# Optimization experiments

Hardware: AMD Instinct MI355X
Metric: run time of the kernel (lower is better)

Reference implementation:

```python
import jax, jax.numpy as jnp
import numpy as np

B, T, V, E, H, O = 64, 512, 32000, 512, 512, 1

def setup_inputs() -> dict:
    key = jax.random.key(0)
    ks = jax.random.split(key, 6)
    s = 0.02  # small init scale to keep gates unsaturated
    return {
        "input_words": jax.random.randint(ks[0], (B, T), 0, V, dtype=jnp.int64),
        "emb": jax.random.normal(ks[1], (V, E), jnp.float32) * s,
        "Wi": jax.random.normal(ks[2], (E, 4 * H), jnp.float32) * s,
        "bi": jnp.zeros((4 * H,), jnp.float32),
        "Wh": jax.random.normal(ks[3], (H, 4 * H), jnp.float32) * s,
        "bh": jnp.zeros((4 * H,), jnp.float32),
        "W_lstm": jax.random.normal(ks[4], (H, H), jnp.float32) * s,
        "b_lstm": jnp.zeros((H,), jnp.float32),
        "W_att": jax.random.normal(ks[5], (2 * H, O), jnp.float32) * s,
        "b_att": jnp.zeros((O,), jnp.float32),
    }


def reference(input_words, emb, Wi, bi, Wh, bh, W_lstm, b_lstm, W_att, b_att):
    batch, seq_len = input_words.shape
    x = emb[input_words]                                  # [B,T,E]
    # precompute all input-side gate projections (r,f,g,o stacked)
    xp = jnp.einsum('bte,eg->tbg', x, Wi) + bi            # [T,B,4H]

    h0 = jnp.zeros((batch, H), xp.dtype)
    c0 = jnp.zeros((batch, H), xp.dtype)

    def step(carry, xp_t):
        h, c = carry
        gates = xp_t + h @ Wh + bh                        # [B,4H]
        r, f, g, o = jnp.split(gates, 4, axis=-1)
        rt = jax.nn.sigmoid(r)
        ft = jax.nn.sigmoid(f)
        gt = jnp.tanh(g)
        ot = jax.nn.sigmoid(o)
        c = ft * c + rt * gt
        h = ot * jnp.tanh(c)
        return (h, c), h

    (h, c), hs = jax.lax.scan(step, (h0, c0), xp)         # hs: [T,B,H]
    outputs = hs.transpose(1, 0, 2)                       # [B,T,H]

    final_hidden = h @ W_lstm + b_lstm                    # [B,H]
    score = jnp.einsum('bth,bh->bt', outputs, final_hidden)
    dist = jax.nn.softmax(score, axis=-1)                 # torch Softmax() -> dim=1 on 2D
    att = jnp.einsum('bth,bt->bh', outputs, dist)
    out = jnp.concatenate([final_hidden, att], axis=1) @ W_att + b_att
    return jax.nn.sigmoid(out), h
```

## Files before the change

kernel.cpp:

```cpp
#include <hip/hip_runtime.h>
#include <hip/hip_bf16.h>

#define BB 64
#define TT 512
#define EE 512
#define HH 512
#define G4 2048
#define VV 32000
#define NWG 64

typedef float f32x4 __attribute__((ext_vector_type(4)));
typedef short s16x8 __attribute__((ext_vector_type(8)));
typedef unsigned short u16x8 __attribute__((ext_vector_type(8)));

__device__ __forceinline__ unsigned short f2bf(float x) {
    __hip_bfloat16 h = __float2bfloat16(x);
    return *(unsigned short*)&h;
}
__device__ __forceinline__ float b2f(unsigned short u) {
    return __uint_as_float(((unsigned)u) << 16);
}

__global__ __launch_bounds__(256) void c_bf16(const float* __restrict__ in,
                                              unsigned short* __restrict__ out, int n4) {
    int i = blockIdx.x * 256 + threadIdx.x;
    if (i < n4) {
        float4 v = ((const float4*)in)[i];
        ushort4 o;
        o.x = f2bf(v.x); o.y = f2bf(v.y); o.z = f2bf(v.z); o.w = f2bf(v.w);
        ((ushort4*)out)[i] = o;
    }
}

__global__ __launch_bounds__(256) void c_wT(const float* __restrict__ in,
                                            unsigned short* __restrict__ out) {
    __shared__ float tile[32][33];
    int gx = blockIdx.x * 32;
    int ky = blockIdx.y * 32;
    int tx = threadIdx.x & 31, ty = threadIdx.x >> 5;
    #pragma unroll
    for (int i = 0; i < 32; i += 8)
        tile[ty + i][tx] = in[(size_t)(ky + ty + i) * G4 + gx + tx];
    __syncthreads();
    #pragma unroll
    for (int i = 0; i < 32; i += 8)
        out[(size_t)(gx + ty + i) * HH + ky + tx] = f2bf(tile[tx][ty + i]);
}

__global__ void zero_flags(int* __restrict__ f) { f[threadIdx.x] = 0; }

__global__ __launch_bounds__(256) void k1_mfma(const int* __restrict__ words,
                                               const unsigned short* __restrict__ embb,
                                               const unsigned short* __restrict__ WiT,
                                               const float* __restrict__ bi,
                                               unsigned short* __restrict__ xp) {
    __shared__ short As[128 * 40];
    __shared__ short Bs[128 * 40];
    __shared__ int wrow[128];
    const int tid = threadIdx.x;
    const int bx = blockIdx.x;
    const int by = blockIdx.y;
    if (tid < 128) {
        int m = by * 128 + tid;
        wrow[tid] = words[(m & 63) * TT + (m >> 6)];
    }
    const int lane = tid & 63;
    const int wv = tid >> 6;
    const int wm = (wv >> 1) * 64, wn = (wv & 1) * 64;
    const int fr = lane & 15, fg = lane >> 4;
    f32x4 acc[4][4] = {};
    float bv[4];
    #pragma unroll
    for (int ni = 0; ni < 4; ++ni) bv[ni] = bi[bx * 128 + wn + ni * 16 + fr];
    const int r0 = tid >> 2, sg = tid & 3;
    const int r1 = r0 + 64;
    __syncthreads();
    s16x8 a0, a1, b0, b1;
    a0 = *(const s16x8*)&embb[(size_t)wrow[r0] * EE + sg * 8];
    a1 = *(const s16x8*)&embb[(size_t)wrow[r1] * EE + sg * 8];
    b0 = *(const s16x8*)&WiT[(size_t)(bx * 128 + r0) * EE + sg * 8];
    b1 = *(const s16x8*)&WiT[(size_t)(bx * 128 + r1) * EE + sg * 8];
    for (int kt = 0; kt < 16; ++kt) {
        __syncthreads();
        *(s16x8*)&As[r0 * 40 + sg * 8] = a0;
        *(s16x8*)&As[r1 * 40 + sg * 8] = a1;
        *(s16x8*)&Bs[r0 * 40 + sg * 8] = b0;
        *(s16x8*)&Bs[r1 * 40 + sg * 8] = b1;
        __syncthreads();
        if (kt < 15) {
            const int k0 = (kt + 1) * 32;
            a0 = *(const s16x8*)&embb[(size_t)wrow[r0] * EE + k0 + sg * 8];
            a1 = *(const s16x8*)&embb[(size_t)wrow[r1] * EE + k0 + sg * 8];
            b0 = *(const s16x8*)&WiT[(size_t)(bx * 128 + r0) * EE + k0 + sg * 8];
            b1 = *(const s16x8*)&WiT[(size_t)(bx * 128 + r1) * EE + k0 + sg * 8];
        }
        s16x8 af[4], bf_[4];
        #pragma unroll
        for (int i = 0; i < 4; ++i) {
            af[i]  = *(const s16x8*)&As[(wm + i * 16 + fr) * 40 + fg * 8];
            bf_[i] = *(const s16x8*)&Bs[(wn + i * 16 + fr) * 40 + fg * 8];
        }
        #pragma unroll
        for (int mi = 0; mi < 4; ++mi)
            #pragma unroll
            for (int ni = 0; ni < 4; ++ni)
                acc[mi][ni] = __builtin_amdgcn_mfma_f32_16x16x32_bf16(
                    af[mi], bf_[ni], acc[mi][ni], 0, 0, 0);
        __syncthreads();
    }
    #pragma unroll
    for (int mi = 0; mi < 4; ++mi) {
        #pragma unroll
        for (int ni = 0; ni < 4; ++ni) {
            int n = bx * 128 + wn + ni * 16 + fr;
            #pragma unroll
            for (int r = 0; r < 4; ++r) {
                int m = by * 128 + wm + mi * 16 + fg * 4 + r;
                xp[(size_t)m * G4 + n] = f2bf(acc[mi][ni][r] + bv[ni]);
            }
        }
    }
}

__global__ __launch_bounds__(256) void k2_persistent(
        const unsigned short* __restrict__ WhT,
        const unsigned short* __restrict__ xp,
        const float* __restrict__ bh,
        unsigned short* __restrict__ hs,
        int* __restrict__ flags) {
    __shared__ short Wl[32 * 520];
    const int wg = blockIdx.x;
    const int tid = threadIdx.x;
    const int lane = tid & 63, wv = tid >> 6;
    const int fr = lane & 15, fg = lane >> 4;
    const int u0 = wg * 8;
    for (int i = tid; i < 32 * 64; i += 256) {
        int n = i >> 6, kc = i & 63;
        int col = (n >> 3) * HH + u0 + (n & 7);
        *(s16x8*)&Wl[n * 520 + kc * 8] = *(const s16x8*)&WhT[(size_t)col * HH + kc * 8];
    }
    const int col0 = ((fr >> 3) ? HH : 0) + u0 + (fr & 7);
    const int col1 = ((fr >> 3) ? 3 * HH : 2 * HH) + u0 + (fr & 7);
    const float bh0 = bh[col0], bh1 = bh[col1];
    const int wb = wv * 16;
    float cst[4] = {0.f, 0.f, 0.f, 0.f};
    unsigned short xq0[4], xq1[4];
    {
        const unsigned short* xrow = xp + ((size_t)(wb + fg * 4)) * G4;
        #pragma unroll
        for (int r = 0; r < 4; ++r) {
            xq0[r] = xrow[(size_t)r * G4 + col0];
            xq1[r] = xrow[(size_t)r * G4 + col1];
        }
    }
    __syncthreads();
    for (int t = 0; t < TT; ++t) {
        f32x4 acc0 = {0.f, 0.f, 0.f, 0.f}, acc1 = {0.f, 0.f, 0.f, 0.f};
        if (t > 0) {
            while (1) {
                int v = __hip_atomic_load(&flags[wv * 64 + lane], __ATOMIC_RELAXED,
                                          __HIP_MEMORY_SCOPE_AGENT);
                if (__all(v >= t)) break;
            }
            asm volatile("" ::: "memory");
            const s16x8* hrow = (const s16x8*)
                (hs + ((size_t)(t - 1) * BB + wb + fr) * HH + fg * 8);
            s16x8 a[16];
            #pragma unroll
            for (int kt = 0; kt < 16; ++kt) a[kt] = hrow[kt * 4];
            __builtin_amdgcn_sched_barrier(0);
            #pragma unroll
            for (int kt = 0; kt < 16; ++kt) {
                s16x8 b0 = *(const s16x8*)&Wl[fr * 520 + kt * 32 + fg * 8];
                s16x8 b1 = *(const s16x8*)&Wl[(16 + fr) * 520 + kt * 32 + fg * 8];
                acc0 = __builtin_amdgcn_mfma_f32_16x16x32_bf16(a[kt], b0, acc0, 0, 0, 0);
                acc1 = __builtin_amdgcn_mfma_f32_16x16x32_bf16(a[kt], b1, acc1, 0, 0, 0);
            }
        }
        float g0[4], g1[4];
        #pragma unroll
        for (int r = 0; r < 4; ++r) {
            g0[r] = acc0[r] + b2f(xq0[r]) + bh0;
            g1[r] = acc1[r] + b2f(xq1[r]) + bh1;
        }
        #pragma unroll
        for (int r = 0; r < 4; ++r) {
            float rv = g0[r], fv = __shfl_xor(g0[r], 8);
            float gv = g1[r], ov = __shfl_xor(g1[r], 8);
            float rt = 1.f / (1.f + __expf(-rv));
            float ft = 1.f / (1.f + __expf(-fv));
            float gt = tanhf(gv);
            float ot = 1.f / (1.f + __expf(-ov));
            cst[r] = ft * cst[r] + rt * gt;
            float h = ot * tanhf(cst[r]);
            unsigned short hu = f2bf(h);
            unsigned short pu = (unsigned short)__shfl_xor((int)hu, 1);
            if (fr < 8 && (fr & 1) == 0) {
                unsigned int packed = (unsigned)hu | ((unsigned)pu << 16);
                unsigned int* dst = (unsigned int*)
                    (hs + ((size_t)t * BB + wb + fg * 4 + r) * HH + u0 + fr);
                __hip_atomic_store(dst, packed, __ATOMIC_RELAXED,
                                   __HIP_MEMORY_SCOPE_AGENT);
            }
        }
        asm volatile("s_waitcnt vmcnt(0)" ::: "memory");
        __hip_atomic_store(&flags[wv * 64 + wg], t + 1, __ATOMIC_RELAXED,
                           __HIP_MEMORY_SCOPE_AGENT);
        {
            int tn = (t + 1 < TT) ? (t + 1) : t;
            const unsigned short* xrow = xp + ((size_t)tn * BB + wb + fg * 4) * G4;
            #pragma unroll
            for (int r = 0; r < 4; ++r) {
                xq0[r] = xrow[(size_t)r * G4 + col0];
                xq1[r] = xrow[(size_t)r * G4 + col1];
            }
        }
    }
}

__global__ __launch_bounds__(512) void k3_fh(const unsigned short* __restrict__ hs,
                                             const float* __restrict__ Wl,
                                             const float* __restrict__ bl,
                                             float* __restrict__ fh) {
    const int b = blockIdx.x;
    const int j = threadIdx.x;
    __shared__ float hl[512];
    hl[j] = b2f(hs[((size_t)(TT - 1) * BB + b) * HH + j]);
    __syncthreads();
    float acc = bl[j];
    #pragma unroll 8
    for (int k = 0; k < HH; ++k) acc += hl[k] * Wl[(size_t)k * HH + j];
    fh[(size_t)b * HH + j] = acc;
}

__global__ __launch_bounds__(256) void k4_att(const unsigned short* __restrict__ hs,
                                              const float* __restrict__ fh,
                                              const float* __restrict__ Wa,
                                              const float* __restrict__ ba,
                                              float* __restrict__ out) {
    const int b = blockIdx.x;
    const int tid = threadIdx.x;
    const int lane = tid & 63, w = tid >> 6;
    __shared__ float scores[512];
    __shared__ float attl[512];
    __shared__ float red[8];
    float fr[8];
    *(float4*)&fr[0] = *(const float4*)&fh[(size_t)b * HH + lane * 8];
    *(float4*)&fr[4] = *(const float4*)&fh[(size_t)b * HH + lane * 8 + 4];
    for (int t = w; t < TT; t += 4) {
        const unsigned short* hrow = hs + ((size_t)t * BB + b) * HH + lane * 8;
        u16x8 hv = *(const u16x8*)hrow;
        float v = 0.f;
        #pragma unroll
        for (int i = 0; i < 8; ++i) v += b2f(hv[i]) * fr[i];
        #pragma unroll
        for (int o = 32; o; o >>= 1) v += __shfl_xor(v, o);
        if (lane == 0) scores[t] = v;
    }
    __syncthreads();
    float s0 = scores[tid], s1 = scores[tid + 256];
    float m = fmaxf(s0, s1);
    #pragma unroll
    for (int o = 32; o; o >>= 1) m = fmaxf(m, __shfl_xor(m, o));
    if (lane == 0) red[w] = m;
    __syncthreads();
    m = fmaxf(fmaxf(red[0], red[1]), fmaxf(red[2], red[3]));
    float e0 = __expf(s0 - m), e1 = __expf(s1 - m);
    float s = e0 + e1;
    #pragma unroll
    for (int o = 32; o; o >>= 1) s += __shfl_xor(s, o);
    if (lane == 0) red[4 + w] = s;
    __syncthreads();
    s = red[4] + red[5] + red[6] + red[7];
    float inv = 1.f / s;
    scores[tid] = e0 * inv;
    scores[tid + 256] = e1 * inv;
    __syncthreads();
    float a0 = 0.f, a1 = 0.f;
    for (int t = 0; t < TT; ++t) {
        float d = scores[t];
        const unsigned short* hrow = hs + ((size_t)t * BB + b) * HH;
        a0 += d * b2f(hrow[tid]);
        a1 += d * b2f(hrow[tid + 256]);
    }
    attl[tid] = a0; attl[tid + 256] = a1;
    const unsigned short* hlast = hs + ((size_t)(TT - 1) * BB + b) * HH;
    out[64 + (size_t)b * HH + tid] = b2f(hlast[tid]);
    out[64 + (size_t)b * HH + tid + 256] = b2f(hlast[tid + 256]);
    __syncthreads();
    float p = fh[(size_t)b * HH + tid] * Wa[tid]
            + fh[(size_t)b * HH + tid + 256] * Wa[tid + 256]
            + attl[tid] * Wa[512 + tid]
            + attl[tid + 256] * Wa[768 + tid];
    #pragma unroll
    for (int o = 32; o; o >>= 1) p += __shfl_xor(p, o);
    if (lane == 0) red[w] = p;
    __syncthreads();
    if (tid == 0) {
        float v = red[0] + red[1] + red[2] + red[3] + ba[0];
        out[b] = 1.f / (1.f + __expf(-v));
    }
}

extern "C" void kernel_launch(void* const* d_in, const int* in_sizes, int n_in,
                              void* d_out, int out_size, void* d_ws, size_t ws_size,
                              hipStream_t stream) {
    const int*   words = (const int*)d_in[0];
    const float* emb   = (const float*)d_in[1];
    const float* Wi    = (const float*)d_in[2];
    const float* bi    = (const float*)d_in[3];
    const float* Wh    = (const float*)d_in[4];
    const float* bh    = (const float*)d_in[5];
    const float* Wl    = (const float*)d_in[6];
    const float* blst  = (const float*)d_in[7];
    const float* Wa    = (const float*)d_in[8];
    const float* ba    = (const float*)d_in[9];
    float* out = (float*)d_out;

    char* ws = (char*)d_ws;
    size_t off = 0;
    unsigned short* emb_bf = (unsigned short*)(ws + off); off += (size_t)VV * EE * 2;
    unsigned short* WiT    = (unsigned short*)(ws + off); off += (size_t)G4 * HH * 2;
    unsigned short* WhT    = (unsigned short*)(ws + off); off += (size_t)G4 * HH * 2;
    unsigned short* xp     = (unsigned short*)(ws + off); off += (size_t)TT * BB * G4 * 2;
    unsigned short* hs     = (unsigned short*)(ws + off); off += (size_t)TT * BB * HH * 2;
    float* fh    = (float*)(ws + off); off += (size_t)BB * HH * 4;
    int*   flags = (int*)(ws + off);   off += 4 * NWG * sizeof(int);
    (void)ws_size; (void)in_sizes; (void)n_in; (void)out_size;

    c_bf16<<<(VV * EE / 4 + 255) / 256, 256, 0, stream>>>(emb, emb_bf, VV * EE / 4);
    c_wT<<<dim3(64, 16), 256, 0, stream>>>(Wi, WiT);
    c_wT<<<dim3(64, 16), 256, 0, stream>>>(Wh, WhT);
    zero_flags<<<1, 4 * NWG, 0, stream>>>(flags);
    k1_mfma<<<dim3(16, 256), 256, 0, stream>>>(words, emb_bf, WiT, bi, xp);
    k2_persistent<<<NWG, 256, 0, stream>>>(WhT, xp, bh, hs, flags);
    k3_fh<<<64, 512, 0, stream>>>(hs, Wl, blst, fh);
    k4_att<<<64, 256, 0, stream>>>(hs, fh, Wa, ba, out);
}
```

Measured before the change: 2.754 ms.

## Replace store-drain before flag with sentinel-bit validation of hidden-state reads

Forces the low mantissa bit of every stored bf16 hidden value to 1 and zeroes the hs buffer beforehand, so readers can detect unwritten data by checking those bits. This lets the producer drop the vmcnt(0) wait before publishing its step flag; consumers instead re-read with atomic loads until all sentinel bits are set. The aim is to remove store-completion latency from the serial recurrence critical path. In exchange it perturbs every hidden value by one bf16 ulp, adds a full-buffer zeroing kernel, and relies on relaxed ordering between the data stores and the flag store.

```diff
diff --git a/kernel.cpp b/kernel.cpp
--- a/kernel.cpp
+++ b/kernel.cpp
@@ -48,6 +48,10 @@
 }
 
 __global__ void zero_flags(int* __restrict__ f) { f[threadIdx.x] = 0; }
+
+__global__ __launch_bounds__(256) void k_zero(uint4* __restrict__ p) {
+    p[(size_t)blockIdx.x * 256 + threadIdx.x] = make_uint4(0, 0, 0, 0);
+}
 
 __global__ __launch_bounds__(256) void k1_mfma(const int* __restrict__ words,
                                                const unsigned short* __restrict__ embb,
@@ -163,12 +167,42 @@
                 if (__all(v >= t)) break;
             }
             asm volatile("" ::: "memory");
-            const s16x8* hrow = (const s16x8*)
-                (hs + ((size_t)(t - 1) * BB + wb + fr) * HH + fg * 8);
+            const unsigned short* hbase =
+                hs + ((size_t)(t - 1) * BB + wb + fr) * HH + fg * 8;
+            const s16x8* hrow = (const s16x8*)hbase;
             s16x8 a[16];
             #pragma unroll
             for (int kt = 0; kt < 16; ++kt) a[kt] = hrow[kt * 4];
             __builtin_amdgcn_sched_barrier(0);
+            {
+                unsigned andv = 0x00010001u;
+                #pragma unroll
+                for (int kt = 0; kt < 16; ++kt) {
+                    union { s16x8 v; unsigned u[4]; } c; c.v = a[kt];
+                    andv &= c.u[0] & c.u[1] & c.u[2] & c.u[3];
+                }
+                bool ok = (andv & 0x00010001u) == 0x00010001u;
+                while (!__all(ok)) {
+                    const unsigned long long* hq = (const unsigned long long*)hbase;
+                    #pragma unroll
+                    for (int kt = 0; kt < 16; ++kt) {
+                        unsigned long long lo = __hip_atomic_load(
+                            &hq[kt * 8], __ATOMIC_RELAXED, __HIP_MEMORY_SCOPE_AGENT);
+                        unsigned long long hi = __hip_atomic_load(
+                            &hq[kt * 8 + 1], __ATOMIC_RELAXED, __HIP_MEMORY_SCOPE_AGENT);
+                        union { unsigned long long q[2]; s16x8 v; } u2;
+                        u2.q[0] = lo; u2.q[1] = hi;
+                        a[kt] = u2.v;
+                    }
+                    unsigned av = 0x00010001u;
+                    #pragma unroll
+                    for (int kt = 0; kt < 16; ++kt) {
+                        union { s16x8 v; unsigned u[4]; } c; c.v = a[kt];
+                        av &= c.u[0] & c.u[1] & c.u[2] & c.u[3];
+                    }
+                    ok = (av & 0x00010001u) == 0x00010001u;
+                }
+            }
             #pragma unroll
             for (int kt = 0; kt < 16; ++kt) {
                 s16x8 b0 = *(const s16x8*)&Wl[fr * 520 + kt * 32 + fg * 8];
@@ -193,7 +227,7 @@
             float ot = 1.f / (1.f + __expf(-ov));
             cst[r] = ft * cst[r] + rt * gt;
             float h = ot * tanhf(cst[r]);
-            unsigned short hu = f2bf(h);
+            unsigned short hu = (unsigned short)(f2bf(h) | 1u);
             unsigned short pu = (unsigned short)__shfl_xor((int)hu, 1);
             if (fr < 8 && (fr & 1) == 0) {
                 unsigned int packed = (unsigned)hu | ((unsigned)pu << 16);
@@ -203,7 +237,7 @@
                                    __HIP_MEMORY_SCOPE_AGENT);
             }
         }
-        asm volatile("s_waitcnt vmcnt(0)" ::: "memory");
+        asm volatile("" ::: "memory");
         __hip_atomic_store(&flags[wv * 64 + wg], t + 1, __ATOMIC_RELAXED,
                            __HIP_MEMORY_SCOPE_AGENT);
         {
@@ -332,6 +366,7 @@
     c_wT<<<dim3(64, 16), 256, 0, stream>>>(Wi, WiT);
     c_wT<<<dim3(64, 16), 256, 0, stream>>>(Wh, WhT);
     zero_flags<<<1, 4 * NWG, 0, stream>>>(flags);
+    k_zero<<<(int)(((size_t)TT * BB * HH * 2 / 16 + 255) / 256), 256, 0, stream>>>((uint4*)hs);
     k1_mfma<<<dim3(16, 256), 256, 0, stream>>>(words, emb_bf, WiT, bi, xp);
     k2_persistent<<<NWG, 256, 0, stream>>>(WhT, xp, bh, hs, flags);
     k3_fh<<<64, 512, 0, stream>>>(hs, Wl, blst, fh);
```

Measured after the change: 2.934 ms. 1.07x slower.

## Shrink persistent LSTM recurrence to 16 workgroups with 32 hidden units each

Applied to the files above, without the earlier changes.

The persistent recurrent kernel now runs on 16 workgroups instead of 64, and each one owns 32 hidden units (128 gate columns) rather than 8. The Wh slice moves to dynamic shared memory of about 130KB, and each wave issues 8 MFMAs per k-step instead of 2. The aim is to cut the per-timestep cross-workgroup flag polling and synchronisation latency by having fewer participants. In exchange, each workgroup does four times more serial MFMA and activation work per step, and fewer compute units are used.

```diff
diff --git a/kernel.cpp b/kernel.cpp
--- a/kernel.cpp
+++ b/kernel.cpp
@@ -7,7 +7,7 @@
 #define HH 512
 #define G4 2048
 #define VV 32000
-#define NWG 64
+#define NWG 16
 
 typedef float f32x4 __attribute__((ext_vector_type(4)));
 typedef short s16x8 __attribute__((ext_vector_type(8)));
@@ -122,43 +122,60 @@
     }
 }
 
-__global__ __launch_bounds__(256) void k2_persistent(
+__global__ __launch_bounds__(256, 1) void k2_persistent(
         const unsigned short* __restrict__ WhT,
         const unsigned short* __restrict__ xp,
         const float* __restrict__ bh,
         unsigned short* __restrict__ hs,
         int* __restrict__ flags) {
-    __shared__ short Wl[32 * 520];
+    extern __shared__ short Wl[];
     const int wg = blockIdx.x;
     const int tid = threadIdx.x;
     const int lane = tid & 63, wv = tid >> 6;
     const int fr = lane & 15, fg = lane >> 4;
-    const int u0 = wg * 8;
-    for (int i = tid; i < 32 * 64; i += 256) {
+    const int u0 = wg * 32;
+    for (int i = tid; i < 128 * 64; i += 256) {
         int n = i >> 6, kc = i & 63;
-        int col = (n >> 3) * HH + u0 + (n & 7);
-        *(s16x8*)&Wl[n * 520 + kc * 8] = *(const s16x8*)&WhT[(size_t)col * HH + kc * 8];
-    }
-    const int col0 = ((fr >> 3) ? HH : 0) + u0 + (fr & 7);
-    const int col1 = ((fr >> 3) ? 3 * HH : 2 * HH) + u0 + (fr & 7);
-    const float bh0 = bh[col0], bh1 = bh[col1];
+        int cg = n >> 4, f2 = n & 15;
+        int gate = ((cg >> 2) << 1) + (f2 >> 3);
+        int uo = (cg & 3) * 8 + (f2 & 7);
+        int gcol = gate * HH + u0 + uo;
+        *(s16x8*)&Wl[n * 520 + kc * 8] = *(const s16x8*)&WhT[(size_t)gcol * HH + kc * 8];
+    }
+    int col0[4], col1[4];
+    float bh0[4], bh1[4];
+    #pragma unroll
+    for (int cg = 0; cg < 4; ++cg) {
+        col0[cg] = (fr >> 3) * HH + u0 + cg * 8 + (fr & 7);
+        col1[cg] = (2 + (fr >> 3)) * HH + u0 + cg * 8 + (fr & 7);
+        bh0[cg] = bh[col0[cg]];
+        bh1[cg] = bh[col1[cg]];
+    }
     const int wb = wv * 16;
-    float cst[4] = {0.f, 0.f, 0.f, 0.f};
-    unsigned short xq0[4], xq1[4];
+    float cst[4][4];
+    #pragma unroll
+    for (int cg = 0; cg < 4; ++cg)
+        #pragma unroll
+        for (int r = 0; r < 4; ++r) cst[cg][r] = 0.f;
+    unsigned short xq0[4][4], xq1[4][4];
     {
         const unsigned short* xrow = xp + ((size_t)(wb + fg * 4)) * G4;
         #pragma unroll
-        for (int r = 0; r < 4; ++r) {
-            xq0[r] = xrow[(size_t)r * G4 + col0];
-            xq1[r] = xrow[(size_t)r * G4 + col1];
-        }
+        for (int cg = 0; cg < 4; ++cg)
+            #pragma unroll
+            for (int r = 0; r < 4; ++r) {
+                xq0[cg][r] = xrow[(size_t)r * G4 + col0[cg]];
+                xq1[cg][r] = xrow[(size_t)r * G4 + col1[cg]];
+            }
     }
     __syncthreads();
     for (int t = 0; t < TT; ++t) {
-        f32x4 acc0 = {0.f, 0.f, 0.f, 0.f}, acc1 = {0.f, 0.f, 0.f, 0.f};
+        f32x4 acc[8];
+        #pragma unroll
+        for (int cg = 0; cg < 8; ++cg) acc[cg] = (f32x4){0.f, 0.f, 0.f, 0.f};
         if (t > 0) {
             while (1) {
-                int v = __hip_atomic_load(&flags[wv * 64 + lane], __ATOMIC_RELAXED,
+                int v = __hip_atomic_load(&flags[wv * 16 + (lane & 15)], __ATOMIC_RELAXED,
                                           __HIP_MEMORY_SCOPE_AGENT);
                 if (__all(v >= t)) break;
             }
@@ -171,49 +188,51 @@
             __builtin_amdgcn_sched_barrier(0);
             #pragma unroll
             for (int kt = 0; kt < 16; ++kt) {
-                s16x8 b0 = *(const s16x8*)&Wl[fr * 520 + kt * 32 + fg * 8];
-                s16x8 b1 = *(const s16x8*)&Wl[(16 + fr) * 520 + kt * 32 + fg * 8];
-                acc0 = __builtin_amdgcn_mfma_f32_16x16x32_bf16(a[kt], b0, acc0, 0, 0, 0);
-                acc1 = __builtin_amdgcn_mfma_f32_16x16x32_bf16(a[kt], b1, acc1, 0, 0, 0);
-            }
-        }
-        float g0[4], g1[4];
-        #pragma unroll
-        for (int r = 0; r < 4; ++r) {
-            g0[r] = acc0[r] + b2f(xq0[r]) + bh0;
-            g1[r] = acc1[r] + b2f(xq1[r]) + bh1;
-        }
-        #pragma unroll
-        for (int r = 0; r < 4; ++r) {
-            float rv = g0[r], fv = __shfl_xor(g0[r], 8);
-            float gv = g1[r], ov = __shfl_xor(g1[r], 8);
-            float rt = 1.f / (1.f + __expf(-rv));
-            float ft = 1.f / (1.f + __expf(-fv));
-            float gt = tanhf(gv);
-            float ot = 1.f / (1.f + __expf(-ov));
-            cst[r] = ft * cst[r] + rt * gt;
-            float h = ot * tanhf(cst[r]);
-            unsigned short hu = f2bf(h);
-            unsigned short pu = (unsigned short)__shfl_xor((int)hu, 1);
-            if (fr < 8 && (fr & 1) == 0) {
-                unsigned int packed = (unsigned)hu | ((unsigned)pu << 16);
-                unsigned int* dst = (unsigned int*)
-                    (hs + ((size_t)t * BB + wb + fg * 4 + r) * HH + u0 + fr);
-                __hip_atomic_store(dst, packed, __ATOMIC_RELAXED,
-                                   __HIP_MEMORY_SCOPE_AGENT);
+                #pragma unroll
+                for (int cg = 0; cg < 8; ++cg) {
+                    s16x8 b = *(const s16x8*)&Wl[(cg * 16 + fr) * 520 + kt * 32 + fg * 8];
+                    acc[cg] = __builtin_amdgcn_mfma_f32_16x16x32_bf16(a[kt], b, acc[cg], 0, 0, 0);
+                }
+            }
+        }
+        #pragma unroll
+        for (int cg = 0; cg < 4; ++cg) {
+            #pragma unroll
+            for (int r = 0; r < 4; ++r) {
+                float g0 = acc[cg][r] + b2f(xq0[cg][r]) + bh0[cg];
+                float g1 = acc[cg + 4][r] + b2f(xq1[cg][r]) + bh1[cg];
+                float rv = g0, fv = __shfl_xor(g0, 8);
+                float gv = g1, ov = __shfl_xor(g1, 8);
+                float rt = 1.f / (1.f + __expf(-rv));
+                float ft = 1.f / (1.f + __expf(-fv));
+                float gt = tanhf(gv);
+                float ot = 1.f / (1.f + __expf(-ov));
+                cst[cg][r] = ft * cst[cg][r] + rt * gt;
+                float h = ot * tanhf(cst[cg][r]);
+                unsigned short hu = f2bf(h);
+                unsigned short pu = (unsigned short)__shfl_xor((int)hu, 1);
+                if (fr < 8 && (fr & 1) == 0) {
+                    unsigned int packed = (unsigned)hu | ((unsigned)pu << 16);
+                    unsigned int* dst = (unsigned int*)
+                        (hs + ((size_t)t * BB + wb + fg * 4 + r) * HH + u0 + cg * 8 + fr);
+                    __hip_atomic_store(dst, packed, __ATOMIC_RELAXED,
+                                       __HIP_MEMORY_SCOPE_AGENT);
+                }
             }
         }
         asm volatile("s_waitcnt vmcnt(0)" ::: "memory");
-        __hip_atomic_store(&flags[wv * 64 + wg], t + 1, __ATOMIC_RELAXED,
+        __hip_atomic_store(&flags[wv * 16 + wg], t + 1, __ATOMIC_RELAXED,
                            __HIP_MEMORY_SCOPE_AGENT);
         {
             int tn = (t + 1 < TT) ? (t + 1) : t;
             const unsigned short* xrow = xp + ((size_t)tn * BB + wb + fg * 4) * G4;
             #pragma unroll
-            for (int r = 0; r < 4; ++r) {
-                xq0[r] = xrow[(size_t)r * G4 + col0];
-                xq1[r] = xrow[(size_t)r * G4 + col1];
-            }
+            for (int cg = 0; cg < 4; ++cg)
+                #pragma unroll
+                for (int r = 0; r < 4; ++r) {
+                    xq0[cg][r] = xrow[(size_t)r * G4 + col0[cg]];
+                    xq1[cg][r] = xrow[(size_t)r * G4 + col1[cg]];
+                }
         }
     }
 }
@@ -333,7 +352,7 @@
     c_wT<<<dim3(64, 16), 256, 0, stream>>>(Wh, WhT);
     zero_flags<<<1, 4 * NWG, 0, stream>>>(flags);
     k1_mfma<<<dim3(16, 256), 256, 0, stream>>>(words, emb_bf, WiT, bi, xp);
-    k2_persistent<<<NWG, 256, 0, stream>>>(WhT, xp, bh, hs, flags);
+    k2_persistent<<<NWG, 256, 128 * 520 * sizeof(short), stream>>>(WhT, xp, bh, hs, flags);
     k3_fh<<<64, 512, 0, stream>>>(hs, Wl, blst, fh);
     k4_att<<<64, 256, 0, stream>>>(hs, fh, Wa, ba, out);
 }
```

After: 4.904 ms. 78.0% more time.
